# Performance work log

Hardware: AMD Instinct MI355X
Metric: run time of the kernel (lower is better)

## Reference

```python
import jax, jax.numpy as jnp
import numpy as np

NI = 512
HEADS = 8
DH = NI // HEADS  # 64 = attn_chans
EPS = 1e-5

def _ln(x, g, b):
    mu = jnp.mean(x, axis=-1, keepdims=True)
    var = jnp.var(x, axis=-1, keepdims=True)
    return (x - mu) * jax.lax.rsqrt(var + EPS) * g + b

def setup_inputs() -> dict:
    key = jax.random.key(0)
    ks = jax.random.split(key, 5)
    n, c, h, w = 8, NI, 32, 32
    return {
        "x": jax.random.normal(ks[0], (n, c, h, w), jnp.float32),
        "query_x": jax.random.normal(ks[1], (n, c, h, w), jnp.float32),
        "q_ln_g": jnp.ones((c,), jnp.float32),
        "q_ln_b": jnp.zeros((c,), jnp.float32),
        "q_w": jax.random.normal(ks[2], (c, c), jnp.float32) / np.sqrt(c),
        "q_b": jnp.zeros((c,), jnp.float32),
        "kv_ln_g": jnp.ones((c,), jnp.float32),
        "kv_ln_b": jnp.zeros((c,), jnp.float32),
        "kv_w": jax.random.normal(ks[3], (c, 2 * c), jnp.float32) / np.sqrt(c),
        "kv_b": jnp.zeros((2 * c,), jnp.float32),
        "proj_w": jax.random.normal(ks[4], (c, c), jnp.float32) / np.sqrt(c),
        "proj_b": jnp.zeros((c,), jnp.float32),
    }

def reference(x, query_x, q_ln_g, q_ln_b, q_w, q_b, kv_ln_g, kv_ln_b, kv_w, kv_b, proj_w, proj_b):
    n, c, h, w = x.shape
    s = h * w
    xs = x.reshape(n, c, s).transpose(0, 2, 1)        # (n, s, c)
    qx = query_x.reshape(n, c, s).transpose(0, 2, 1)  # (n, s, c)
    q_proj = _ln(qx, q_ln_g, q_ln_b) @ q_w + q_b        # (n, s, c)
    kv = _ln(xs, kv_ln_g, kv_ln_b) @ kv_w + kv_b        # (n, s, 2c)
    cat = jnp.concatenate([q_proj, kv], axis=-1)        # (n, s, 3c)
    # rearrange 'n s (h d3)' with h=HEADS, d3 = 3*DH, then chunk into q,k,v
    cat = cat.reshape(n, s, HEADS, 3 * DH).transpose(0, 2, 1, 3)  # (n, H, s, 3d)
    q, k, v = jnp.split(cat, 3, axis=-1)                # each (n, H, s, d)
    scale = jnp.sqrt(jnp.asarray(DH, q.dtype))          # sqrt(ni/nheads)
    scores = jnp.einsum('nhqd,nhkd->nhqk', q, k) / scale
    attn = jax.nn.softmax(scores, axis=-1)
    o = jnp.einsum('nhqk,nhkd->nhqd', attn, v)          # (n, H, s, d)
    o = o.transpose(0, 2, 1, 3).reshape(n, s, c)        # (n, s, c)
    o = o @ proj_w + proj_b
    return o.transpose(0, 2, 1).reshape(n, c, h, w)
```

## Files before the change

### kernel.cpp

```cpp
#include <hip/hip_runtime.h>
#include <math.h>

namespace {

constexpr int S = 1024;
constexpr int C = 512;
constexpr int NBATCH = 8;
constexpr int RTOT = NBATCH * S;
constexpr int HEADS = 8;
constexpr int DH = 64;

typedef __attribute__((ext_vector_type(8))) short bf16x8;
typedef __attribute__((ext_vector_type(4))) float f32x4;
typedef __attribute__((ext_vector_type(16))) float f32x16;
typedef unsigned short u16;
typedef unsigned int u32;

__device__ __forceinline__ u16 f2bf(float x) {
  union { float f; u32 u; } v; v.f = x;
  u32 r = v.u + 0x7FFF + ((v.u >> 16) & 1);
  return (u16)(r >> 16);
}
__device__ __forceinline__ float bf2f(u16 b) {
  union { u32 u; float f; } v; v.u = (u32)b << 16; return v.f;
}
__device__ __forceinline__ u32 cvtpk(float a, float b) {
  u32 r;
  asm("v_cvt_pk_bf16_f32 %0, %1, %2" : "=v"(r) : "v"(a), "v"(b));
  return r;
}
__device__ __forceinline__ float fexp2(float x) {
  float r;
  asm("v_exp_f32 %0, %1" : "=v"(r) : "v"(x));
  return r;
}
__device__ __forceinline__ float fmax3(float a, float b, float c) {
  return fmaxf(fmaxf(a, b), c);
}
__device__ __forceinline__ void gl_lds16(const void* g, void* l) {
  auto gp = (const __attribute__((address_space(1))) u32*)g;
  auto lp = (__attribute__((address_space(3))) u32*)l;
  __builtin_amdgcn_global_load_lds(gp, lp, 16, 0, 0);
}

__global__ void ln_fused(const float* __restrict__ x, const float* __restrict__ qx,
                         const float* __restrict__ gx, const float* __restrict__ bx,
                         const float* __restrict__ gq, const float* __restrict__ bq,
                         u16* __restrict__ Xkv, u16* __restrict__ Xq) {
  __shared__ float Ssum[8][32], Ssq[8][32];
  __shared__ float mu_s[32], rs_s[32];
  __shared__ float T[2][32][65];
  int t = threadIdx.x;
  int si0 = blockIdx.x * 32;
  int isq = blockIdx.y & 1, n = blockIdx.y >> 1;
  const float* in = isq ? qx : x;
  const float* g  = isq ? gq : gx;
  const float* be = isq ? bq : bx;
  u16* out = isq ? Xq : Xkv;

  {
    int sl = t & 31, cg = t >> 5;
    const float* p = in + ((size_t)n * C + cg * 64) * S + si0 + sl;
    float s = 0.f, sq = 0.f;
#pragma unroll 8
    for (int c = 0; c < 64; c++) { float v = p[(size_t)c * S]; s += v; sq += v * v; }
    Ssum[cg][sl] = s; Ssq[cg][sl] = sq;
  }
  __syncthreads();
  if (t < 32) {
    float ss = 0.f, q2 = 0.f;
#pragma unroll
    for (int i = 0; i < 8; i++) { ss += Ssum[i][t]; q2 += Ssq[i][t]; }
    float m = ss * (1.0f / C);
    float var = q2 * (1.0f / C) - m * m;
    mu_s[t] = m; rs_s[t] = rsqrtf(var + 1e-5f);
  }
  __syncthreads();

  int si4 = (t & 7) * 4, cl = t >> 3;
  float4 mu4 = *(const float4*)&mu_s[si4];
  float4 rs4 = *(const float4*)&rs_s[si4];
  int wsl = t >> 3, wc8 = (t & 7) * 8;

  for (int it = 0; it < 8; it++) {
    int c0 = it * 64, b = it & 1;
#pragma unroll
    for (int i = 0; i < 2; i++) {
      int c = c0 + cl + i * 32;
      float4 v = *(const float4*)&in[((size_t)n * C + c) * S + si0 + si4];
      float gg = g[c], bb = be[c];
      T[b][si4 + 0][cl + i * 32] = (v.x - mu4.x) * rs4.x * gg + bb;
      T[b][si4 + 1][cl + i * 32] = (v.y - mu4.y) * rs4.y * gg + bb;
      T[b][si4 + 2][cl + i * 32] = (v.z - mu4.z) * rs4.z * gg + bb;
      T[b][si4 + 3][cl + i * 32] = (v.w - mu4.w) * rs4.w * gg + bb;
    }
    __syncthreads();
    u16 pk[8];
#pragma unroll
    for (int j = 0; j < 8; j++) pk[j] = f2bf(T[b][wsl][wc8 + j]);
    *(uint4*)&out[((size_t)(n * S + si0 + wsl)) * C + c0 + wc8] = *(const uint4*)pk;
  }
}

__global__ void prep_w(const float* __restrict__ qw, const float* __restrict__ kvw,
                       const float* __restrict__ pw,
                       u16* __restrict__ Wtq, u16* __restrict__ Wtkv,
                       u16* __restrict__ Wph) {
  int z = blockIdx.z;
  int N = (z == 1) ? 1024 : 512;
  int col0 = blockIdx.y * 64;
  if (col0 >= N) return;
  int k0 = blockIdx.x * 64;
  const float* W = (z == 0) ? qw : (z == 1) ? kvw : pw;
  __shared__ float T[64][65];
  int t = threadIdx.x;
  int kl = t >> 4, c4 = (t & 15) * 4;
#pragma unroll
  for (int i = 0; i < 4; i++) {
    float4 v = *(const float4*)&W[(size_t)(k0 + kl + i * 16) * N + col0 + c4];
    T[kl + i * 16][c4 + 0] = v.x; T[kl + i * 16][c4 + 1] = v.y;
    T[kl + i * 16][c4 + 2] = v.z; T[kl + i * 16][c4 + 3] = v.w;
  }
  __syncthreads();
#pragma unroll
  for (int p = 0; p < 2; p++) {
    int cl = (t >> 3) + p * 32, k8 = (t & 7) * 8;
    u16 hi[8];
#pragma unroll
    for (int j = 0; j < 8; j++) hi[j] = f2bf(T[k8 + j][cl]);
    size_t o = (size_t)(col0 + cl) * 512 + k0 + k8;
    if (z == 0) *(uint4*)&Wtq[o] = *(const uint4*)hi;
    else if (z == 1) *(uint4*)&Wtkv[o] = *(const uint4*)hi;
    else *(uint4*)&Wph[o] = *(const uint4*)hi;
  }
}

__global__ __launch_bounds__(256, 4) void gemm_qkv(
    const u16* __restrict__ Xq, const u16* __restrict__ Xkv,
    const u16* __restrict__ Wtq, const u16* __restrict__ Wtkv,
    const float* __restrict__ q_b, const float* __restrict__ kv_b,
    u16* __restrict__ Qb, u16* __restrict__ Kb, u16* __restrict__ Vt) {
  __shared__ __attribute__((aligned(16))) u16 As[128 * 64];
  __shared__ __attribute__((aligned(16))) u16 Bs[128 * 64];
  int t = threadIdx.x, wid = t >> 6, lane = t & 63, lr = lane & 15, lg = lane >> 4;
  int colb = blockIdx.x;
  const u16* A; const u16* Wt; const float* bias; int ch0;
  if (colb < 4) { A = Xq;  Wt = Wtq  + (size_t)colb * 128 * 512;       bias = q_b  + colb * 128;       ch0 = colb * 128; }
  else          { A = Xkv; Wt = Wtkv + (size_t)(colb - 4) * 128 * 512; bias = kv_b + (colb - 4) * 128; ch0 = 512 + (colb - 4) * 128; }
  int row0 = blockIdx.y * 128;
  int wr = wid >> 1, wc = wid & 1;
  f32x4 acc[4][4];
#pragma unroll
  for (int m = 0; m < 4; m++)
#pragma unroll
    for (int n = 0; n < 4; n++) acc[m][n] = (f32x4){0.f, 0.f, 0.f, 0.f};

  for (int k0 = 0; k0 < 512; k0 += 64) {
    __syncthreads();
#pragma unroll
    for (int it = 0; it < 4; it++) {
      int chunk = (wid * 4 + it) * 64 + lane;
      int r = chunk >> 3, sg = chunk & 7;
      gl_lds16(A + (size_t)(row0 + r) * 512 + k0 + ((sg ^ (r & 7)) * 8),
               (char*)As + (size_t)chunk * 16);
    }
#pragma unroll
    for (int it = 0; it < 4; it++) {
      int chunk = (wid * 4 + it) * 64 + lane;
      int r = chunk >> 3, sg = chunk & 7;
      gl_lds16(Wt + (size_t)r * 512 + k0 + ((sg ^ (r & 7)) * 8),
               (char*)Bs + (size_t)chunk * 16);
    }
    __syncthreads();
#pragma unroll
    for (int kk = 0; kk < 2; kk++) {
      bf16x8 bfr[4];
#pragma unroll
      for (int n = 0; n < 4; n++) {
        int col = wc * 64 + n * 16 + lr;
        bfr[n] = *(const bf16x8*)((const char*)Bs + col * 128 + (((kk * 4 + lg) ^ (col & 7)) << 4));
      }
#pragma unroll
      for (int m = 0; m < 4; m++) {
        int row = wr * 64 + m * 16 + lr;
        bf16x8 af = *(const bf16x8*)((const char*)As + row * 128 + (((kk * 4 + lg) ^ (row & 7)) << 4));
#pragma unroll
        for (int n = 0; n < 4; n++)
          acc[m][n] = __builtin_amdgcn_mfma_f32_16x16x32_bf16(af, bfr[n], acc[m][n], 0, 0, 0);
      }
    }
  }
#pragma unroll
  for (int m = 0; m < 4; m++)
#pragma unroll
    for (int n = 0; n < 4; n++) {
      int colg = wc * 64 + n * 16 + lr;
      int ch = ch0 + colg;
      int h = ch / 192, role = (ch >> 6) % 3, d = ch & 63;
      float bs = bias[colg];
      float qsc = (role == 0) ? 0.18033688f : 1.0f;
      int growb = row0 + wr * 64 + m * 16 + lg * 4;
      int nn = growb >> 10, ssi0 = growb & (S - 1);
      size_t nh = (size_t)(nn * HEADS + h);
      if (role == 2) {
        u16 pk[4];
#pragma unroll
        for (int r = 0; r < 4; r++) pk[r] = f2bf(acc[m][n][r] + bs);
        *(uint2*)&Vt[(nh * DH + d) * S + ssi0] = *(const uint2*)pk;
      } else {
        u16* dst = (role == 0) ? Qb : Kb;
#pragma unroll
        for (int r = 0; r < 4; r++)
          dst[(nh * S + ssi0 + r) * DH + d] = f2bf((acc[m][n][r] + bs) * qsc);
      }
    }
}

__global__ __launch_bounds__(256, 4) void gemm_proj(
    const u16* __restrict__ Aob, const u16* __restrict__ Wh,
    const float* __restrict__ bias, float* __restrict__ out) {
  __shared__ __attribute__((aligned(16))) u16 As[128 * 64];
  __shared__ __attribute__((aligned(16))) u16 Bh[64 * 64];
  int t = threadIdx.x, wid = t >> 6, lane = t & 63, lr = lane & 15, lg = lane >> 4;
  int ch0 = blockIdx.x * 64, row0 = blockIdx.y * 128;
  int wc = wid & 1, wr = wid >> 1;
  f32x4 acc[2][4];
#pragma unroll
  for (int m = 0; m < 2; m++)
#pragma unroll
    for (int n = 0; n < 4; n++) acc[m][n] = (f32x4){0.f, 0.f, 0.f, 0.f};

  for (int k0 = 0; k0 < 512; k0 += 64) {
    __syncthreads();
#pragma unroll
    for (int it = 0; it < 4; it++) {
      int idx = (wid * 4 + it) * 64 + lane;
      int r = idx >> 3, sg = idx & 7;
      gl_lds16(Aob + (size_t)(row0 + r) * 512 + k0 + ((sg ^ (r & 7)) * 8),
               (char*)As + (wid * 4 + it) * 1024);
    }
#pragma unroll
    for (int it = 0; it < 2; it++) {
      int idx = (wid * 2 + it) * 64 + lane;
      int r = idx >> 3, sg = idx & 7;
      gl_lds16(Wh + (size_t)(ch0 + r) * 512 + k0 + ((sg ^ (r & 7)) * 8),
               (char*)Bh + (wid * 2 + it) * 1024);
    }
    __syncthreads();
#pragma unroll
    for (int kk = 0; kk < 2; kk++) {
      bf16x8 ar[4];
#pragma unroll
      for (int n = 0; n < 4; n++) {
        int row = wr * 64 + n * 16 + lr;
        ar[n] = *(const bf16x8*)((const char*)As + row * 128 + (((kk * 4 + lg) ^ (row & 7)) << 4));
      }
#pragma unroll
      for (int m = 0; m < 2; m++) {
        int ch = wc * 32 + m * 16 + lr;
        bf16x8 bh = *(const bf16x8*)((const char*)Bh + ch * 128 + (((kk * 4 + lg) ^ (ch & 7)) << 4));
#pragma unroll
        for (int n = 0; n < 4; n++)
          acc[m][n] = __builtin_amdgcn_mfma_f32_16x16x32_bf16(bh, ar[n], acc[m][n], 0, 0, 0);
      }
    }
  }
#pragma unroll
  for (int m = 0; m < 2; m++)
#pragma unroll
    for (int n = 0; n < 4; n++) {
      int rowg = row0 + wr * 64 + n * 16 + lr;
      int nn = rowg >> 10, ssi = rowg & (S - 1);
#pragma unroll
      for (int r = 0; r < 4; r++) {
        int ch = ch0 + wc * 32 + m * 16 + lg * 4 + r;
        out[((size_t)nn * C + ch) * S + ssi] = acc[m][n][r] + bias[ch];
      }
    }
}

constexpr int KVB = 64;

__global__ __launch_bounds__(256, 4) void attn_kernel(
    const u16* __restrict__ Qbf, const u16* __restrict__ Kbf,
    const u16* __restrict__ Vtb, u16* __restrict__ Obf) {
  __shared__ __attribute__((aligned(16))) u16 Ks[2][KVB * DH];
  __shared__ __attribute__((aligned(16))) u16 Vs[2][DH * KVB];

  int tid = threadIdx.x;
  int wave = tid >> 6, lane = tid & 63;
  int lq = lane & 31, hi = lane >> 5;
  int qg = wave & 1, kg = wave >> 1;
  int w = (blockIdx.x & 7) * 128 + (blockIdx.x >> 3);
  int qt = w & 15, nh = w >> 4;
  const u16* Qg = Qbf + (size_t)nh * S * DH;
  const u16* Kg = Kbf + (size_t)nh * S * DH;
  const u16* Vg = Vtb + (size_t)nh * DH * S;

  int qrow = qt * 64 + qg * 32 + lq;
  bf16x8 qf[4];
#pragma unroll
  for (int ks = 0; ks < 4; ks++)
    qf[ks] = *(const bf16x8*)(Qg + (size_t)qrow * DH + ks * 16 + hi * 8);

  bf16x8 ones;
#pragma unroll
  for (int i = 0; i < 8; i++) ones[i] = (short)0x3F80;

  f32x16 oa0 = {}, oa1 = {}, lacc = {};
  float m_run = -1e30f;

  int e0i = tid, e1i = tid + 256;
  int r0 = e0i >> 3, sg0 = e0i & 7, r1 = e1i >> 3, sg1 = e1i & 7;
  char* kd0 = (char*)&Ks[0][0] + (e0i & ~63) * 16;
  char* kd1 = (char*)&Ks[0][0] + (e1i & ~63) * 16;
  char* vd0 = (char*)&Vs[0][0] + (e0i & ~63) * 16;
  char* vd1 = (char*)&Vs[0][0] + (e1i & ~63) * 16;

#define STAGE(kb, b)                                                             \
  do {                                                                           \
    gl_lds16(Kg + (size_t)((kb) * KVB + r0) * 64 + ((sg0 ^ (r0 & 7)) * 8),       \
             kd0 + (b) * (KVB * DH * 2));                                        \
    gl_lds16(Kg + (size_t)((kb) * KVB + r1) * 64 + ((sg1 ^ (r1 & 7)) * 8),       \
             kd1 + (b) * (KVB * DH * 2));                                        \
    gl_lds16(Vg + (size_t)r0 * S + (kb) * KVB + ((sg0 ^ (r0 & 7)) * 8),          \
             vd0 + (b) * (KVB * DH * 2));                                        \
    gl_lds16(Vg + (size_t)r1 * S + (kb) * KVB + ((sg1 ^ (r1 & 7)) * 8),          \
             vd1 + (b) * (KVB * DH * 2));                                        \
  } while (0)

  STAGE(0, 0);

  for (int kb = 0; kb < S / KVB; kb++) {
    int cur = kb & 1;
    __syncthreads();
    if (kb + 1 < S / KVB) STAGE(kb + 1, cur ^ 1);

    const char* Kc = (const char*)&Ks[cur][0];
    const char* Vc = (const char*)&Vs[cur][0];

    f32x16 sc = {};
#pragma unroll
    for (int ks = 0; ks < 4; ks++) {
      int sg = ks * 2 + hi;
      bf16x8 kf = *(const bf16x8*)(Kc + (kg * 32 + lq) * 128 + ((sg ^ (lq & 7)) << 4));
      sc = __builtin_amdgcn_mfma_f32_32x32x16_bf16(kf, qf[ks], sc, 0, 0, 0);
    }

    bf16x8 vfr[2][2];
#pragma unroll
    for (int kk = 0; kk < 2; kk++) {
      int sg = kg * 4 + kk * 2 + hi;
      vfr[kk][0] = *(const bf16x8*)(Vc + lq * 128 + ((sg ^ (lq & 7)) << 4));
      vfr[kk][1] = *(const bf16x8*)(Vc + (32 + lq) * 128 + ((sg ^ (lq & 7)) << 4));
    }

    float g0 = fmax3(sc[0], sc[1], sc[2]);
    float g1 = fmax3(sc[3], sc[4], sc[5]);
    float g2 = fmax3(sc[6], sc[7], sc[8]);
    float g3 = fmax3(sc[9], sc[10], sc[11]);
    float g4 = fmax3(sc[12], sc[13], sc[14]);
    float pmax = fmax3(fmax3(g0, g1, g2), fmaxf(g3, g4), sc[15]);
    pmax = fmaxf(pmax, __shfl_xor(pmax, 32));

    if (!__all(pmax <= m_run + 11.5f)) {
      float mnew = fmaxf(m_run, pmax);
      float corr = fexp2(m_run - mnew);
      m_run = mnew;
      lacc[0] *= corr;
#pragma unroll
      for (int r = 0; r < 16; r++) { oa0[r] *= corr; oa1[r] *= corr; }
    }

#pragma unroll
    for (int r = 0; r < 16; r++) sc[r] = fexp2(sc[r] - m_run);

    u32 c[8];
    c[0] = cvtpk(sc[0],  sc[1]);  c[1] = cvtpk(sc[2],  sc[3]);
    c[2] = cvtpk(sc[4],  sc[5]);  c[3] = cvtpk(sc[6],  sc[7]);
    c[4] = cvtpk(sc[8],  sc[9]);  c[5] = cvtpk(sc[10], sc[11]);
    c[6] = cvtpk(sc[12], sc[13]); c[7] = cvtpk(sc[14], sc[15]);
    asm("v_permlane32_swap_b32 %0, %1" : "+v"(c[0]), "+v"(c[2]));
    asm("v_permlane32_swap_b32 %0, %1" : "+v"(c[1]), "+v"(c[3]));
    asm("v_permlane32_swap_b32 %0, %1" : "+v"(c[4]), "+v"(c[6]));
    asm("v_permlane32_swap_b32 %0, %1" : "+v"(c[5]), "+v"(c[7]));

#pragma unroll
    for (int kk = 0; kk < 2; kk++) {
      union { u32 u[4]; bf16x8 v; } pu;
      pu.u[0] = c[kk * 4 + 0]; pu.u[1] = c[kk * 4 + 1];
      pu.u[2] = c[kk * 4 + 2]; pu.u[3] = c[kk * 4 + 3];
      lacc = __builtin_amdgcn_mfma_f32_32x32x16_bf16(ones, pu.v, lacc, 0, 0, 0);
      oa0 = __builtin_amdgcn_mfma_f32_32x32x16_bf16(vfr[kk][0], pu.v, oa0, 0, 0, 0);
      oa1 = __builtin_amdgcn_mfma_f32_32x32x16_bf16(vfr[kk][1], pu.v, oa1, 0, 0, 0);
    }
  }
#undef STAGE

  float l_run = lacc[0];
  __syncthreads();
  float* exO = (float*)&Ks[0][0];
  float* exS = (float*)&Vs[0][0];
  if (kg) {
    float* o = exO + qg * 2048;
#pragma unroll
    for (int r = 0; r < 16; r++) {
      o[r * 64 + lane] = oa0[r];
      o[(16 + r) * 64 + lane] = oa1[r];
    }
    exS[qg * 128 + lane] = m_run;
    exS[qg * 128 + 64 + lane] = l_run;
  }
  __syncthreads();
  if (!kg) {
    float* o = exO + qg * 2048;
    float m2 = exS[qg * 128 + lane];
    float l2 = exS[qg * 128 + 64 + lane];
    float m = fmaxf(m_run, m2);
    float f0 = fexp2(m_run - m), f2 = fexp2(m2 - m);
    l_run = l_run * f0 + l2 * f2;
#pragma unroll
    for (int r = 0; r < 16; r++) {
      oa0[r] = oa0[r] * f0 + o[r * 64 + lane] * f2;
      oa1[r] = oa1[r] * f0 + o[(16 + r) * 64 + lane] * f2;
    }
    int n = nh >> 3, h = nh & 7;
    float lf = 1.0f / l_run;
    u16* orow = Obf + ((size_t)n * S + qrow) * C + h * DH;
#pragma unroll
    for (int rq = 0; rq < 4; rq++) {
      int d0 = rq * 8 + 4 * hi;
      uint2 w0, w1;
      w0.x = cvtpk(oa0[rq * 4 + 0] * lf, oa0[rq * 4 + 1] * lf);
      w0.y = cvtpk(oa0[rq * 4 + 2] * lf, oa0[rq * 4 + 3] * lf);
      w1.x = cvtpk(oa1[rq * 4 + 0] * lf, oa1[rq * 4 + 1] * lf);
      w1.y = cvtpk(oa1[rq * 4 + 2] * lf, oa1[rq * 4 + 3] * lf);
      *(uint2*)(orow + d0) = w0;
      *(uint2*)(orow + 32 + d0) = w1;
    }
  }
}

}

extern "C" void kernel_launch(void* const* d_in, const int* in_sizes, int n_in,
                              void* d_out, int out_size, void* d_ws, size_t ws_size,
                              hipStream_t stream) {
  const float* x       = (const float*)d_in[0];
  const float* qx      = (const float*)d_in[1];
  const float* q_ln_g  = (const float*)d_in[2];
  const float* q_ln_b  = (const float*)d_in[3];
  const float* q_w     = (const float*)d_in[4];
  const float* q_b     = (const float*)d_in[5];
  const float* kv_ln_g = (const float*)d_in[6];
  const float* kv_ln_b = (const float*)d_in[7];
  const float* kv_w    = (const float*)d_in[8];
  const float* kv_b    = (const float*)d_in[9];
  const float* proj_w  = (const float*)d_in[10];
  const float* proj_b  = (const float*)d_in[11];
  float* out = (float*)d_out;

  u16* u = (u16*)d_ws;
  u16* Xkv  = u;                u += (size_t)RTOT * C;
  u16* Xq   = u;                u += (size_t)RTOT * C;
  u16* Wtq  = u;                u += (size_t)C * C;
  u16* Wtkv = u;                u += (size_t)2 * C * C;
  u16* Wph  = u;                u += (size_t)C * C;
  u16* Qb   = u;                u += (size_t)NBATCH * HEADS * S * DH;
  u16* Kb   = u;                u += (size_t)NBATCH * HEADS * S * DH;
  u16* Vt   = u;                u += (size_t)NBATCH * HEADS * S * DH;
  u16* Obf  = u;

  hipLaunchKernelGGL(ln_fused, dim3(S / 32, 2 * NBATCH), dim3(256), 0, stream,
                     x, qx, kv_ln_g, kv_ln_b, q_ln_g, q_ln_b, Xkv, Xq);
  hipLaunchKernelGGL(prep_w, dim3(8, 16, 3), dim3(256), 0, stream,
                     q_w, kv_w, proj_w, Wtq, Wtkv, Wph);
  hipLaunchKernelGGL(gemm_qkv, dim3(12, RTOT / 128), dim3(256), 0, stream,
                     Xq, Xkv, Wtq, Wtkv, q_b, kv_b, Qb, Kb, Vt);
  hipLaunchKernelGGL(attn_kernel, dim3(1024), dim3(256), 0, stream,
                     Qb, Kb, Vt, Obf);
  hipLaunchKernelGGL(gemm_proj, dim3(C / 64, RTOT / 128), dim3(256), 0, stream,
                     Obf, Wph, proj_b, out);
}
```

Measured before the change: 87.06 us.

## Merge LayerNorm and weight prep kernels, remap GEMM blocks for XCD locality

Combines the LayerNorm/transposition kernel and the weight-conversion kernel into one launch, with a block-index split and shared LDS buffer, removing one kernel launch and the gap between the two. Both GEMMs now use a 1D grid whose block ids are remapped so that consecutive blocks on the same XCD (bid&7) share rows or weight columns, aiming for better L2 reuse. The remap assumes 8 XCDs with round-robin dispatch. The merged kernel's LDS footprint is sized for the larger LayerNorm branch, which may lower occupancy for the weight-prep blocks.

```diff
diff --git a/kernel.cpp b/kernel.cpp
--- a/kernel.cpp
+++ b/kernel.cpp
@@ -43,95 +43,105 @@
   __builtin_amdgcn_global_load_lds(gp, lp, 16, 0, 0);
 }
 
-__global__ void ln_fused(const float* __restrict__ x, const float* __restrict__ qx,
-                         const float* __restrict__ gx, const float* __restrict__ bx,
-                         const float* __restrict__ gq, const float* __restrict__ bq,
-                         u16* __restrict__ Xkv, u16* __restrict__ Xq) {
-  __shared__ float Ssum[8][32], Ssq[8][32];
-  __shared__ float mu_s[32], rs_s[32];
-  __shared__ float T[2][32][65];
+__global__ void ln_prep(const float* __restrict__ x, const float* __restrict__ qx,
+                        const float* __restrict__ gx, const float* __restrict__ bx,
+                        const float* __restrict__ gq, const float* __restrict__ bq,
+                        u16* __restrict__ Xkv, u16* __restrict__ Xq,
+                        const float* __restrict__ qw, const float* __restrict__ kvw,
+                        const float* __restrict__ pw,
+                        u16* __restrict__ Wtq, u16* __restrict__ Wtkv,
+                        u16* __restrict__ Wph) {
+  __shared__ __attribute__((aligned(16))) float smemf[4736];
+  int bid = blockIdx.x;
   int t = threadIdx.x;
-  int si0 = blockIdx.x * 32;
-  int isq = blockIdx.y & 1, n = blockIdx.y >> 1;
-  const float* in = isq ? qx : x;
-  const float* g  = isq ? gq : gx;
-  const float* be = isq ? bq : bx;
-  u16* out = isq ? Xq : Xkv;
-
-  {
-    int sl = t & 31, cg = t >> 5;
-    const float* p = in + ((size_t)n * C + cg * 64) * S + si0 + sl;
-    float s = 0.f, sq = 0.f;
+
+  if (bid < 512) {
+    float (*Ssum)[32] = (float(*)[32])smemf;
+    float (*Ssq)[32]  = (float(*)[32])(smemf + 256);
+    float* mu_s = smemf + 512;
+    float* rs_s = smemf + 544;
+    float (*T)[32][65] = (float(*)[32][65])(smemf + 576);
+
+    int si0 = (bid & 31) * 32;
+    int yy = bid >> 5;
+    int isq = yy & 1, n = yy >> 1;
+    const float* in = isq ? qx : x;
+    const float* g  = isq ? gq : gx;
+    const float* be = isq ? bq : bx;
+    u16* out = isq ? Xq : Xkv;
+
+    {
+      int sl = t & 31, cg = t >> 5;
+      const float* p = in + ((size_t)n * C + cg * 64) * S + si0 + sl;
+      float s = 0.f, sq = 0.f;
 #pragma unroll 8
-    for (int c = 0; c < 64; c++) { float v = p[(size_t)c * S]; s += v; sq += v * v; }
-    Ssum[cg][sl] = s; Ssq[cg][sl] = sq;
-  }
-  __syncthreads();
-  if (t < 32) {
-    float ss = 0.f, q2 = 0.f;
-#pragma unroll
-    for (int i = 0; i < 8; i++) { ss += Ssum[i][t]; q2 += Ssq[i][t]; }
-    float m = ss * (1.0f / C);
-    float var = q2 * (1.0f / C) - m * m;
-    mu_s[t] = m; rs_s[t] = rsqrtf(var + 1e-5f);
-  }
-  __syncthreads();
-
-  int si4 = (t & 7) * 4, cl = t >> 3;
-  float4 mu4 = *(const float4*)&mu_s[si4];
-  float4 rs4 = *(const float4*)&rs_s[si4];
-  int wsl = t >> 3, wc8 = (t & 7) * 8;
-
-  for (int it = 0; it < 8; it++) {
-    int c0 = it * 64, b = it & 1;
-#pragma unroll
-    for (int i = 0; i < 2; i++) {
-      int c = c0 + cl + i * 32;
-      float4 v = *(const float4*)&in[((size_t)n * C + c) * S + si0 + si4];
-      float gg = g[c], bb = be[c];
-      T[b][si4 + 0][cl + i * 32] = (v.x - mu4.x) * rs4.x * gg + bb;
-      T[b][si4 + 1][cl + i * 32] = (v.y - mu4.y) * rs4.y * gg + bb;
-      T[b][si4 + 2][cl + i * 32] = (v.z - mu4.z) * rs4.z * gg + bb;
-      T[b][si4 + 3][cl + i * 32] = (v.w - mu4.w) * rs4.w * gg + bb;
-    }
-    __syncthreads();
-    u16 pk[8];
-#pragma unroll
-    for (int j = 0; j < 8; j++) pk[j] = f2bf(T[b][wsl][wc8 + j]);
-    *(uint4*)&out[((size_t)(n * S + si0 + wsl)) * C + c0 + wc8] = *(const uint4*)pk;
-  }
-}
-
-__global__ void prep_w(const float* __restrict__ qw, const float* __restrict__ kvw,
-                       const float* __restrict__ pw,
-                       u16* __restrict__ Wtq, u16* __restrict__ Wtkv,
-                       u16* __restrict__ Wph) {
-  int z = blockIdx.z;
-  int N = (z == 1) ? 1024 : 512;
-  int col0 = blockIdx.y * 64;
-  if (col0 >= N) return;
-  int k0 = blockIdx.x * 64;
-  const float* W = (z == 0) ? qw : (z == 1) ? kvw : pw;
-  __shared__ float T[64][65];
-  int t = threadIdx.x;
-  int kl = t >> 4, c4 = (t & 15) * 4;
-#pragma unroll
-  for (int i = 0; i < 4; i++) {
-    float4 v = *(const float4*)&W[(size_t)(k0 + kl + i * 16) * N + col0 + c4];
-    T[kl + i * 16][c4 + 0] = v.x; T[kl + i * 16][c4 + 1] = v.y;
-    T[kl + i * 16][c4 + 2] = v.z; T[kl + i * 16][c4 + 3] = v.w;
-  }
-  __syncthreads();
-#pragma unroll
-  for (int p = 0; p < 2; p++) {
-    int cl = (t >> 3) + p * 32, k8 = (t & 7) * 8;
-    u16 hi[8];
-#pragma unroll
-    for (int j = 0; j < 8; j++) hi[j] = f2bf(T[k8 + j][cl]);
-    size_t o = (size_t)(col0 + cl) * 512 + k0 + k8;
-    if (z == 0) *(uint4*)&Wtq[o] = *(const uint4*)hi;
-    else if (z == 1) *(uint4*)&Wtkv[o] = *(const uint4*)hi;
-    else *(uint4*)&Wph[o] = *(const uint4*)hi;
+      for (int c = 0; c < 64; c++) { float v = p[(size_t)c * S]; s += v; sq += v * v; }
+      Ssum[cg][sl] = s; Ssq[cg][sl] = sq;
+    }
+    __syncthreads();
+    if (t < 32) {
+      float ss = 0.f, q2 = 0.f;
+#pragma unroll
+      for (int i = 0; i < 8; i++) { ss += Ssum[i][t]; q2 += Ssq[i][t]; }
+      float m = ss * (1.0f / C);
+      float var = q2 * (1.0f / C) - m * m;
+      mu_s[t] = m; rs_s[t] = rsqrtf(var + 1e-5f);
+    }
+    __syncthreads();
+
+    int si4 = (t & 7) * 4, cl = t >> 3;
+    float4 mu4 = *(const float4*)&mu_s[si4];
+    float4 rs4 = *(const float4*)&rs_s[si4];
+    int wsl = t >> 3, wc8 = (t & 7) * 8;
+
+    for (int it = 0; it < 8; it++) {
+      int c0 = it * 64, b = it & 1;
+#pragma unroll
+      for (int i = 0; i < 2; i++) {
+        int c = c0 + cl + i * 32;
+        float4 v = *(const float4*)&in[((size_t)n * C + c) * S + si0 + si4];
+        float gg = g[c], bb = be[c];
+        T[b][si4 + 0][cl + i * 32] = (v.x - mu4.x) * rs4.x * gg + bb;
+        T[b][si4 + 1][cl + i * 32] = (v.y - mu4.y) * rs4.y * gg + bb;
+        T[b][si4 + 2][cl + i * 32] = (v.z - mu4.z) * rs4.z * gg + bb;
+        T[b][si4 + 3][cl + i * 32] = (v.w - mu4.w) * rs4.w * gg + bb;
+      }
+      __syncthreads();
+      u16 pk[8];
+#pragma unroll
+      for (int j = 0; j < 8; j++) pk[j] = f2bf(T[b][wsl][wc8 + j]);
+      *(uint4*)&out[((size_t)(n * S + si0 + wsl)) * C + c0 + wc8] = *(const uint4*)pk;
+    }
+  } else {
+    float (*T)[65] = (float(*)[65])smemf;
+    int pid = bid - 512;
+    int z, k0t, colt;
+    if (pid < 64)       { z = 0;               k0t = pid & 7; colt = pid >> 3; }
+    else if (pid < 192) { z = 1; pid -= 64;    k0t = pid & 7; colt = pid >> 3; }
+    else                { z = 2; pid -= 192;   k0t = pid & 7; colt = pid >> 3; }
+    int N = (z == 1) ? 1024 : 512;
+    int col0 = colt * 64, k0 = k0t * 64;
+    const float* W = (z == 0) ? qw : (z == 1) ? kvw : pw;
+
+    int kl = t >> 4, c4 = (t & 15) * 4;
+#pragma unroll
+    for (int i = 0; i < 4; i++) {
+      float4 v = *(const float4*)&W[(size_t)(k0 + kl + i * 16) * N + col0 + c4];
+      T[kl + i * 16][c4 + 0] = v.x; T[kl + i * 16][c4 + 1] = v.y;
+      T[kl + i * 16][c4 + 2] = v.z; T[kl + i * 16][c4 + 3] = v.w;
+    }
+    __syncthreads();
+#pragma unroll
+    for (int p = 0; p < 2; p++) {
+      int cl = (t >> 3) + p * 32, k8 = (t & 7) * 8;
+      u16 hi[8];
+#pragma unroll
+      for (int j = 0; j < 8; j++) hi[j] = f2bf(T[k8 + j][cl]);
+      size_t o = (size_t)(col0 + cl) * 512 + k0 + k8;
+      if (z == 0) *(uint4*)&Wtq[o] = *(const uint4*)hi;
+      else if (z == 1) *(uint4*)&Wtkv[o] = *(const uint4*)hi;
+      else *(uint4*)&Wph[o] = *(const uint4*)hi;
+    }
   }
 }
 
@@ -143,11 +153,13 @@
   __shared__ __attribute__((aligned(16))) u16 As[128 * 64];
   __shared__ __attribute__((aligned(16))) u16 Bs[128 * 64];
   int t = threadIdx.x, wid = t >> 6, lane = t & 63, lr = lane & 15, lg = lane >> 4;
-  int colb = blockIdx.x;
+  int bid = blockIdx.x;
+  int wg = (bid & 7) * 96 + (bid >> 3);
+  int colb = wg % 12;
+  int row0 = (wg / 12) * 128;
   const u16* A; const u16* Wt; const float* bias; int ch0;
   if (colb < 4) { A = Xq;  Wt = Wtq  + (size_t)colb * 128 * 512;       bias = q_b  + colb * 128;       ch0 = colb * 128; }
   else          { A = Xkv; Wt = Wtkv + (size_t)(colb - 4) * 128 * 512; bias = kv_b + (colb - 4) * 128; ch0 = 512 + (colb - 4) * 128; }
-  int row0 = blockIdx.y * 128;
   int wr = wid >> 1, wc = wid & 1;
   f32x4 acc[4][4];
 #pragma unroll
@@ -222,7 +234,10 @@
   __shared__ __attribute__((aligned(16))) u16 As[128 * 64];
   __shared__ __attribute__((aligned(16))) u16 Bh[64 * 64];
   int t = threadIdx.x, wid = t >> 6, lane = t & 63, lr = lane & 15, lg = lane >> 4;
-  int ch0 = blockIdx.x * 64, row0 = blockIdx.y * 128;
+  int bid = blockIdx.x;
+  int wg = (bid & 7) * 64 + (bid >> 3);
+  int ch0 = (wg % 8) * 64;
+  int row0 = (wg / 8) * 128;
   int wc = wid & 1, wr = wid >> 1;
   f32x4 acc[2][4];
 #pragma unroll
@@ -471,14 +486,13 @@
   u16* Vt   = u;                u += (size_t)NBATCH * HEADS * S * DH;
   u16* Obf  = u;
 
-  hipLaunchKernelGGL(ln_fused, dim3(S / 32, 2 * NBATCH), dim3(256), 0, stream,
-                     x, qx, kv_ln_g, kv_ln_b, q_ln_g, q_ln_b, Xkv, Xq);
-  hipLaunchKernelGGL(prep_w, dim3(8, 16, 3), dim3(256), 0, stream,
+  hipLaunchKernelGGL(ln_prep, dim3(768), dim3(256), 0, stream,
+                     x, qx, kv_ln_g, kv_ln_b, q_ln_g, q_ln_b, Xkv, Xq,
                      q_w, kv_w, proj_w, Wtq, Wtkv, Wph);
-  hipLaunchKernelGGL(gemm_qkv, dim3(12, RTOT / 128), dim3(256), 0, stream,
+  hipLaunchKernelGGL(gemm_qkv, dim3(768), dim3(256), 0, stream,
                      Xq, Xkv, Wtq, Wtkv, q_b, kv_b, Qb, Kb, Vt);
   hipLaunchKernelGGL(attn_kernel, dim3(1024), dim3(256), 0, stream,
                      Qb, Kb, Vt, Obf);
-  hipLaunchKernelGGL(gemm_proj, dim3(C / 64, RTOT / 128), dim3(256), 0, stream,
+  hipLaunchKernelGGL(gemm_proj, dim3(512), dim3(256), 0, stream,
                      Obf, Wph, proj_b, out);
 }
```

Measured after the change: 81.01 us (median of 2 runs). -7.0%, faster.
